# Optimization experiments

Measured on AMD Instinct MI355X. Metric: run time of the kernel, lower is better.

## Reference

```python
import jax, jax.numpy as jnp
import numpy as np

HID = 256

def setup_inputs() -> dict:
    key = jax.random.key(0)
    ks = jax.random.split(key, 16)
    B, N, DIN, DOUT = 256, 1024, 64, 128
    def lin(k, fin, fout):
        kw, kb = jax.random.split(k)
        s = 1.0 / np.sqrt(fin)
        W = jax.random.uniform(kw, (fin, fout), jnp.float32, -s, s)
        b = jax.random.uniform(kb, (fout,), jnp.float32, -s, s)
        return W, b
    x = jax.random.normal(ks[0], (B, N, DIN), jnp.float32)
    mask = jax.random.randint(ks[1], (B, N), 0, 2) > 0
    pw1, pb1 = lin(ks[2], DIN, HID)
    pw2, pb2 = lin(ks[3], HID, HID)
    pw3, pb3 = lin(ks[4], HID, HID)
    rw1, rb1 = lin(ks[5], HID, HID)
    rw2, rb2 = lin(ks[6], HID, HID)
    rw3, rb3 = lin(ks[7], HID, DOUT)
    return dict(x=x, mask=mask, pw1=pw1, pb1=pb1, pw2=pw2, pb2=pb2, pw3=pw3, pb3=pb3,
                rw1=rw1, rb1=rb1, rw2=rw2, rb2=rb2, rw3=rw3, rb3=rb3)

def reference(x, mask, pw1, pb1, pw2, pb2, pw3, pb3, rw1, rb1, rw2, rb2, rw3, rb3):
    # x: [B, N, din], mask: [B, N] bool
    # phi per element (padding elements are zeroed before the pool, matching
    # the torch pack/pad pipeline which only runs phi on valid elements)
    h = jax.nn.relu(jnp.einsum('bnd,dh->bnh', x, pw1) + pb1)
    h = jax.nn.relu(jnp.einsum('bnh,hk->bnk', h, pw2) + pb2)
    h = jnp.einsum('bnh,hk->bnk', h, pw3) + pb3
    m = mask.astype(x.dtype)[..., None]                  # [B, N, 1]
    pooled = jnp.sum(h * m, axis=1)                      # [B, 256]
    o = jax.nn.relu(pooled @ rw1 + rb1)
    o = jax.nn.relu(o @ rw2 + rb2)
    o = o @ rw3 + rb3                                    # [B, dout]
    # rows with zero valid elements get exactly 0 (torch leaves res at 0.0)
    valid = jnp.any(mask, axis=1, keepdims=True)
    return jnp.where(valid, o, jnp.zeros((), dtype=o.dtype))
```

## Files before the change

kernel.cpp:

```cpp
#include <hip/hip_runtime.h>

namespace {
constexpr int NB = 256, NN = 1024, DIN = 64, HID = 256, DOUT = 128;
constexpr int MT = 64;

typedef __attribute__((ext_vector_type(8))) short bf16x8;
typedef __attribute__((ext_vector_type(4))) float f32x4;

constexpr size_t PW1_OFF = 0;
constexpr size_t PW2_OFF = (size_t)DIN * HID * 2;

__device__ inline unsigned short f2bf(float f) {
    union { float f; unsigned u; } v; v.f = f;
    unsigned r = v.u + 0x7FFF + ((v.u >> 16) & 1);
    return (unsigned short)(r >> 16);
}

__global__ void prep(const float* __restrict__ pw1, const float* __restrict__ pw2,
                     unsigned short* __restrict__ w1p, unsigned short* __restrict__ w2p) {
    int i = blockIdx.x * 256 + threadIdx.x;
    if (i < DIN * HID / 8) {
        int s0 = i * 8;
        int k = s0 >> 8, n0 = s0 & 255;
        float4 v0 = *(const float4*)(pw1 + s0);
        float4 v1 = *(const float4*)(pw1 + s0 + 4);
        float vv[8] = {v0.x, v0.y, v0.z, v0.w, v1.x, v1.y, v1.z, v1.w};
        int j = k & 7, quad = (k >> 3) & 3, kk = k >> 5;
#pragma unroll
        for (int e = 0; e < 8; ++e) {
            int n = n0 + e, strip = n >> 4, l15 = n & 15;
            w1p[strip * 1024 + kk * 512 + (quad * 16 + l15) * 8 + j] = f2bf(vv[e]);
        }
    }
    if (i < HID * HID / 8) {
        int s0 = i * 8;
        int k = s0 >> 8, n0 = s0 & 255;
        float4 v0 = *(const float4*)(pw2 + s0);
        float4 v1 = *(const float4*)(pw2 + s0 + 4);
        float vv[8] = {v0.x, v0.y, v0.z, v0.w, v1.x, v1.y, v1.z, v1.w};
        int j = k & 7, quad = (k >> 3) & 3, kk = k >> 5;
#pragma unroll
        for (int e = 0; e < 8; ++e) {
            int n = n0 + e, strip = n >> 4, l15 = n & 15;
            w2p[strip * 4096 + kk * 512 + (quad * 16 + l15) * 8 + j] = f2bf(vv[e]);
        }
    }
}

__device__ inline float4 dotseg(const float* __restrict__ buf, const float* __restrict__ W,
                                int c, int s) {
    const float4* W4 = (const float4*)W;
    float4 acc = make_float4(0.f, 0.f, 0.f, 0.f);
#pragma unroll 8
    for (int i = 0; i < 32; ++i) {
        int k = s * 32 + i;
        float bk = buf[k];
        float4 w = W4[(size_t)k * 64 + c];
        acc.x = fmaf(bk, w.x, acc.x);
        acc.y = fmaf(bk, w.y, acc.y);
        acc.z = fmaf(bk, w.z, acc.z);
        acc.w = fmaf(bk, w.w, acc.w);
    }
    return acc;
}

__launch_bounds__(512, 2)
__global__ void deepset(const float* __restrict__ x, const int* __restrict__ mask,
                        const float* __restrict__ pb1, const float* __restrict__ pb2,
                        const unsigned short* __restrict__ w1p,
                        const unsigned short* __restrict__ w2p,
                        const float* __restrict__ pw3, const float* __restrict__ pb3,
                        const float* __restrict__ rw1, const float* __restrict__ rb1,
                        const float* __restrict__ rw2, const float* __restrict__ rb2,
                        const float* __restrict__ rw3, const float* __restrict__ rb3,
                        float* __restrict__ out)
{
    __shared__ unsigned short xs[2][MT * 64];
    __shared__ unsigned short h1s[MT * 256];
    __shared__ short vlist[NN];
    __shared__ float pooledS[HID];
    __shared__ float part[8][HID];
    __shared__ float bufB[HID], bufC[HID];
    __shared__ int cnt_s;

    const int b = blockIdx.x, t = threadIdx.x;
    const int lane = t & 63, wq = t >> 6;
    const int quad = lane >> 4, l15 = lane & 15;

    if (t == 0) cnt_s = 0;
    __syncthreads();
    if (mask[b * NN + t] != 0)       { int i = atomicAdd(&cnt_s, 1); vlist[i] = (short)t; }
    if (mask[b * NN + t + 512] != 0) { int i = atomicAdd(&cnt_s, 1); vlist[i] = (short)(t + 512); }
    __syncthreads();
    const int cnt = cnt_s;

    const uint4* w1q = (const uint4*)w1p;
    const uint4* w2q = (const uint4*)w2p;
    uint4 w1f[2][2], w2f[8][2];
#pragma unroll
    for (int j = 0; j < 2; ++j) {
        int strip = wq * 2 + j;
#pragma unroll
        for (int kk = 0; kk < 2; ++kk) w1f[kk][j] = w1q[(strip * 2 + kk) * 64 + lane];
#pragma unroll
        for (int kk = 0; kk < 8; ++kk) w2f[kk][j] = w2q[(strip * 8 + kk) * 64 + lane];
    }
    float bias1[2], bias2[2];
#pragma unroll
    for (int j = 0; j < 2; ++j) {
        int c = wq * 32 + j * 16 + l15;
        bias1[j] = pb1[c]; bias2[j] = pb2[c];
    }

    float pool[2] = {0.f, 0.f};
    const float* xb = x + (size_t)b * NN * DIN;
    const int gr = t >> 3, seg8 = t & 7;
    const int xoff = gr * 64 + ((seg8 ^ (gr & 7)) << 3);

    {
        float4 a0 = make_float4(0.f,0.f,0.f,0.f), a1 = a0;
        if (gr < min(MT, cnt)) {
            const float4* p = (const float4*)(xb + (size_t)vlist[gr] * DIN + seg8 * 8);
            a0 = p[0]; a1 = p[1];
        }
        unsigned short tmp[8] = {f2bf(a0.x),f2bf(a0.y),f2bf(a0.z),f2bf(a0.w),
                                 f2bf(a1.x),f2bf(a1.y),f2bf(a1.z),f2bf(a1.w)};
        *(uint4*)&xs[0][xoff] = *(const uint4*)tmp;
    }

    int cur = 0;
    for (int base = 0; base < cnt; base += MT) {
        __syncthreads();

        f32x4 acc[4][2];
#pragma unroll
        for (int f = 0; f < 4; ++f)
#pragma unroll
            for (int j = 0; j < 2; ++j) acc[f][j] = (f32x4){0.f,0.f,0.f,0.f};
#pragma unroll
        for (int kk = 0; kk < 2; ++kk) {
            bf16x8 a[4];
#pragma unroll
            for (int f = 0; f < 4; ++f)
                a[f] = *(const bf16x8*)&xs[cur][(f*16 + l15)*64 + (((kk*4 + quad) ^ (l15 & 7)) << 3)];
#pragma unroll
            for (int j = 0; j < 2; ++j) {
                bf16x8 bw = __builtin_bit_cast(bf16x8, w1f[kk][j]);
#pragma unroll
                for (int f = 0; f < 4; ++f)
                    acc[f][j] = __builtin_amdgcn_mfma_f32_16x16x32_bf16(a[f], bw, acc[f][j], 0, 0, 0);
            }
        }
#pragma unroll
        for (int f = 0; f < 4; ++f)
#pragma unroll
            for (int j = 0; j < 2; ++j) {
                int col = wq * 32 + j * 16 + l15, kb = col >> 3, cl = col & 7;
#pragma unroll
                for (int r = 0; r < 4; ++r) {
                    int row = f * 16 + quad * 4 + r;
                    float h = fmaxf(acc[f][j][r] + bias1[j], 0.f);
                    h1s[row * 256 + ((kb ^ (row & 7)) << 3) + cl] = f2bf(h);
                }
            }

        float4 n0 = make_float4(0.f,0.f,0.f,0.f), n1 = n0;
        const bool hn = (base + MT) < cnt;
        if (hn && gr < cnt - (base + MT)) {
            const float4* p = (const float4*)(xb + (size_t)vlist[base + MT + gr] * DIN + seg8 * 8);
            n0 = p[0]; n1 = p[1];
        }
        __syncthreads();

        f32x4 acc2[4][2];
#pragma unroll
        for (int f = 0; f < 4; ++f)
#pragma unroll
            for (int j = 0; j < 2; ++j) acc2[f][j] = (f32x4){0.f,0.f,0.f,0.f};
#pragma unroll
        for (int kk = 0; kk < 8; ++kk) {
            bf16x8 a[4];
#pragma unroll
            for (int f = 0; f < 4; ++f)
                a[f] = *(const bf16x8*)&h1s[(f*16 + l15)*256 + (((kk*4 + quad) ^ (l15 & 7)) << 3)];
#pragma unroll
            for (int j = 0; j < 2; ++j) {
                bf16x8 bw = __builtin_bit_cast(bf16x8, w2f[kk][j]);
#pragma unroll
                for (int f = 0; f < 4; ++f)
                    acc2[f][j] = __builtin_amdgcn_mfma_f32_16x16x32_bf16(a[f], bw, acc2[f][j], 0, 0, 0);
            }
        }
#pragma unroll
        for (int f = 0; f < 4; ++f)
#pragma unroll
            for (int r = 0; r < 4; ++r) {
                bool v = (base + f * 16 + quad * 4 + r) < cnt;
#pragma unroll
                for (int j = 0; j < 2; ++j) {
                    float h = fmaxf(acc2[f][j][r] + bias2[j], 0.f);
                    pool[j] += v ? h : 0.f;
                }
            }

        if (hn) {
            unsigned short tmp[8] = {f2bf(n0.x),f2bf(n0.y),f2bf(n0.z),f2bf(n0.w),
                                     f2bf(n1.x),f2bf(n1.y),f2bf(n1.z),f2bf(n1.w)};
            *(uint4*)&xs[cur ^ 1][xoff] = *(const uint4*)tmp;
        }
        cur ^= 1;
    }

#pragma unroll
    for (int j = 0; j < 2; ++j) {
        float v = pool[j];
        v += __shfl_xor(v, 16, 64);
        v += __shfl_xor(v, 32, 64);
        if (quad == 0) pooledS[wq * 32 + j * 16 + l15] = v;
    }
    __syncthreads();

    const int c = t & 63, s = t >> 6;
    {
        float4 p = dotseg(pooledS, pw3, c, s);
        ((float4*)part[s])[c] = p;
        __syncthreads();
        if (t < HID) {
            float v = (float)cnt * pb3[t];
#pragma unroll
            for (int g = 0; g < 8; ++g) v += part[g][t];
            bufB[t] = v;
        }
        __syncthreads();
    }
    {
        float4 p = dotseg(bufB, rw1, c, s);
        ((float4*)part[s])[c] = p;
        __syncthreads();
        if (t < HID) {
            float v = rb1[t];
#pragma unroll
            for (int g = 0; g < 8; ++g) v += part[g][t];
            bufC[t] = fmaxf(v, 0.f);
        }
        __syncthreads();
    }
    {
        float4 p = dotseg(bufC, rw2, c, s);
        ((float4*)part[s])[c] = p;
        __syncthreads();
        if (t < HID) {
            float v = rb2[t];
#pragma unroll
            for (int g = 0; g < 8; ++g) v += part[g][t];
            bufB[t] = fmaxf(v, 0.f);
        }
        __syncthreads();
    }
    {
        const int c4 = t & 31, s4 = t >> 5;
        const float4* W4 = (const float4*)rw3;
        float4 acc = make_float4(0.f, 0.f, 0.f, 0.f);
#pragma unroll 8
        for (int i = 0; i < 16; ++i) {
            int k = s4 * 16 + i;
            float bk = bufB[k];
            float4 w = W4[(size_t)k * 32 + c4];
            acc.x = fmaf(bk, w.x, acc.x);
            acc.y = fmaf(bk, w.y, acc.y);
            acc.z = fmaf(bk, w.z, acc.z);
            acc.w = fmaf(bk, w.w, acc.w);
        }
        float* part2 = &part[0][0];
        ((float4*)(part2 + s4 * DOUT))[c4] = acc;
        __syncthreads();
        if (t < DOUT) {
            float v = rb3[t];
#pragma unroll
            for (int g = 0; g < 16; ++g) v += part2[g * DOUT + t];
            out[b * DOUT + t] = (cnt > 0) ? v : 0.f;
        }
    }
}
}

extern "C" void kernel_launch(void* const* d_in, const int* in_sizes, int n_in,
                              void* d_out, int out_size, void* d_ws, size_t ws_size,
                              hipStream_t stream) {
    const float* x    = (const float*)d_in[0];
    const int*   mask = (const int*)  d_in[1];
    const float* pw1  = (const float*)d_in[2];
    const float* pb1  = (const float*)d_in[3];
    const float* pw2  = (const float*)d_in[4];
    const float* pb2  = (const float*)d_in[5];
    const float* pw3  = (const float*)d_in[6];
    const float* pb3  = (const float*)d_in[7];
    const float* rw1  = (const float*)d_in[8];
    const float* rb1  = (const float*)d_in[9];
    const float* rw2  = (const float*)d_in[10];
    const float* rb2  = (const float*)d_in[11];
    const float* rw3  = (const float*)d_in[12];
    const float* rb3  = (const float*)d_in[13];
    float* out = (float*)d_out;

    unsigned short* w1p = (unsigned short*)((char*)d_ws + PW1_OFF);
    unsigned short* w2p = (unsigned short*)((char*)d_ws + PW2_OFF);

    prep<<<dim3(32), dim3(256), 0, stream>>>(pw1, pw2, w1p, w2p);
    deepset<<<dim3(NB), dim3(512), 0, stream>>>(x, mask, pb1, pb2, w1p, w2p,
                                                pw3, pb3, rw1, rb1, rw2, rb2, rw3, rb3, out);
}
```

Baseline: 145.3 us.

## Split per-set phi work across two blocks and move rho to a separate kernel

The fused per-batch kernel is split into a phi_pool kernel launched on a (batch, 2) grid, where each block handles half of the set elements and accumulates pooled sums and counts with global atomics. A separate rho kernel then runs the small MLP on the pooled vectors. Spreading the work over twice as many blocks, with launch bounds raised to 4, is meant to improve occupancy and load balance across the CUs, and prep now writes the weight repack with coalesced vector stores and zeroes the accumulators. The cost is an extra kernel launch, global atomics, and a round trip of the pooled vectors through memory.

```diff
diff --git a/kernel.cpp b/kernel.cpp
--- a/kernel.cpp
+++ b/kernel.cpp
@@ -2,48 +2,202 @@
 
 namespace {
 constexpr int NB = 256, NN = 1024, DIN = 64, HID = 256, DOUT = 128;
+constexpr int SPLIT = 2, CHUNK = NN / SPLIT;
 constexpr int MT = 64;
 
 typedef __attribute__((ext_vector_type(8))) short bf16x8;
 typedef __attribute__((ext_vector_type(4))) float f32x4;
 
-constexpr size_t PW1_OFF = 0;
-constexpr size_t PW2_OFF = (size_t)DIN * HID * 2;
+constexpr size_t POOLED_OFF = 0;
+constexpr size_t CNTS_OFF   = (size_t)NB * HID * 4;
+constexpr size_t PW1_OFF    = CNTS_OFF + (size_t)NB * 4;
+constexpr size_t PW2_OFF    = PW1_OFF + (size_t)DIN * HID * 2;
+constexpr int ZERO_N = NB * HID + NB;
 
 __device__ inline unsigned short f2bf(float f) {
     union { float f; unsigned u; } v; v.f = f;
     unsigned r = v.u + 0x7FFF + ((v.u >> 16) & 1);
     return (unsigned short)(r >> 16);
 }
+__device__ inline unsigned pk2(float lo, float hi) {
+    return (unsigned)f2bf(lo) | ((unsigned)f2bf(hi) << 16);
+}
 
 __global__ void prep(const float* __restrict__ pw1, const float* __restrict__ pw2,
+                     float* __restrict__ zero_base,
                      unsigned short* __restrict__ w1p, unsigned short* __restrict__ w2p) {
     int i = blockIdx.x * 256 + threadIdx.x;
+    if (i < ZERO_N) zero_base[i] = 0.f;
     if (i < DIN * HID / 8) {
-        int s0 = i * 8;
-        int k = s0 >> 8, n0 = s0 & 255;
-        float4 v0 = *(const float4*)(pw1 + s0);
-        float4 v1 = *(const float4*)(pw1 + s0 + 4);
-        float vv[8] = {v0.x, v0.y, v0.z, v0.w, v1.x, v1.y, v1.z, v1.w};
-        int j = k & 7, quad = (k >> 3) & 3, kk = k >> 5;
-#pragma unroll
-        for (int e = 0; e < 8; ++e) {
-            int n = n0 + e, strip = n >> 4, l15 = n & 15;
-            w1p[strip * 1024 + kk * 512 + (quad * 16 + l15) * 8 + j] = f2bf(vv[e]);
-        }
+        int lane = i & 63, kk = (i >> 6) & 1, strip = i >> 7;
+        int kbase = kk * 32 + ((lane >> 4) * 8);
+        int n = strip * 16 + (lane & 15);
+        const float* src = pw1 + (size_t)kbase * HID + n;
+        float v[8];
+#pragma unroll
+        for (int j = 0; j < 8; ++j) v[j] = src[(size_t)j * HID];
+        unsigned o[4] = {pk2(v[0],v[1]), pk2(v[2],v[3]), pk2(v[4],v[5]), pk2(v[6],v[7])};
+        *(uint4*)(w1p + (size_t)i * 8) = *(const uint4*)o;
     }
     if (i < HID * HID / 8) {
-        int s0 = i * 8;
-        int k = s0 >> 8, n0 = s0 & 255;
-        float4 v0 = *(const float4*)(pw2 + s0);
-        float4 v1 = *(const float4*)(pw2 + s0 + 4);
-        float vv[8] = {v0.x, v0.y, v0.z, v0.w, v1.x, v1.y, v1.z, v1.w};
-        int j = k & 7, quad = (k >> 3) & 3, kk = k >> 5;
-#pragma unroll
-        for (int e = 0; e < 8; ++e) {
-            int n = n0 + e, strip = n >> 4, l15 = n & 15;
-            w2p[strip * 4096 + kk * 512 + (quad * 16 + l15) * 8 + j] = f2bf(vv[e]);
-        }
+        int lane = i & 63, kk = (i >> 6) & 7, strip = i >> 9;
+        int kbase = kk * 32 + ((lane >> 4) * 8);
+        int n = strip * 16 + (lane & 15);
+        const float* src = pw2 + (size_t)kbase * HID + n;
+        float v[8];
+#pragma unroll
+        for (int j = 0; j < 8; ++j) v[j] = src[(size_t)j * HID];
+        unsigned o[4] = {pk2(v[0],v[1]), pk2(v[2],v[3]), pk2(v[4],v[5]), pk2(v[6],v[7])};
+        *(uint4*)(w2p + (size_t)i * 8) = *(const uint4*)o;
+    }
+}
+
+__launch_bounds__(512, 4)
+__global__ void phi_pool(const float* __restrict__ x, const int* __restrict__ mask,
+                         const float* __restrict__ pb1, const float* __restrict__ pb2,
+                         const unsigned short* __restrict__ w1p,
+                         const unsigned short* __restrict__ w2p,
+                         float* __restrict__ pooled, int* __restrict__ cnts) {
+    __shared__ unsigned short xs[2][MT * 64];
+    __shared__ unsigned short h1s[MT * 256];
+    __shared__ short vlist[CHUNK];
+    __shared__ int cnt_s;
+
+    const int b = blockIdx.x, sp = blockIdx.y, t = threadIdx.x;
+    const int lane = t & 63, wq = t >> 6;
+    const int quad = lane >> 4, l15 = lane & 15;
+
+    if (t == 0) cnt_s = 0;
+    __syncthreads();
+    {
+        int n = sp * CHUNK + t;
+        if (mask[b * NN + n] != 0) { int i = atomicAdd(&cnt_s, 1); vlist[i] = (short)n; }
+    }
+    __syncthreads();
+    const int cnt = cnt_s;
+    if (t == 0) atomicAdd(&cnts[b], cnt);
+
+    const uint4* w1q = (const uint4*)w1p;
+    const uint4* w2q = (const uint4*)w2p;
+    uint4 w1f[2][2], w2f[8][2];
+#pragma unroll
+    for (int j = 0; j < 2; ++j) {
+        int strip = wq * 2 + j;
+#pragma unroll
+        for (int kk = 0; kk < 2; ++kk) w1f[kk][j] = w1q[(strip * 2 + kk) * 64 + lane];
+#pragma unroll
+        for (int kk = 0; kk < 8; ++kk) w2f[kk][j] = w2q[(strip * 8 + kk) * 64 + lane];
+    }
+    float bias1[2], bias2[2];
+#pragma unroll
+    for (int j = 0; j < 2; ++j) {
+        int c = wq * 32 + j * 16 + l15;
+        bias1[j] = pb1[c]; bias2[j] = pb2[c];
+    }
+
+    float pool[2] = {0.f, 0.f};
+    const float* xb = x + (size_t)b * NN * DIN;
+    const int gr = t >> 3, seg8 = t & 7;
+    const int xoff = gr * 64 + ((seg8 ^ (gr & 7)) << 3);
+
+    {
+        float4 a0 = make_float4(0.f,0.f,0.f,0.f), a1 = a0;
+        if (gr < min(MT, cnt)) {
+            const float4* p = (const float4*)(xb + (size_t)vlist[gr] * DIN + seg8 * 8);
+            a0 = p[0]; a1 = p[1];
+        }
+        unsigned o[4] = {pk2(a0.x,a0.y), pk2(a0.z,a0.w), pk2(a1.x,a1.y), pk2(a1.z,a1.w)};
+        *(uint4*)&xs[0][xoff] = *(const uint4*)o;
+    }
+
+    int cur = 0;
+    for (int base = 0; base < cnt; base += MT) {
+        __syncthreads();
+
+        f32x4 acc[4][2];
+#pragma unroll
+        for (int f = 0; f < 4; ++f)
+#pragma unroll
+            for (int j = 0; j < 2; ++j) acc[f][j] = (f32x4){0.f,0.f,0.f,0.f};
+#pragma unroll
+        for (int kk = 0; kk < 2; ++kk) {
+            bf16x8 a[4];
+#pragma unroll
+            for (int f = 0; f < 4; ++f)
+                a[f] = *(const bf16x8*)&xs[cur][(f*16 + l15)*64 + (((kk*4 + quad) ^ (l15 & 7)) << 3)];
+#pragma unroll
+            for (int j = 0; j < 2; ++j) {
+                bf16x8 bw = __builtin_bit_cast(bf16x8, w1f[kk][j]);
+#pragma unroll
+                for (int f = 0; f < 4; ++f)
+                    acc[f][j] = __builtin_amdgcn_mfma_f32_16x16x32_bf16(a[f], bw, acc[f][j], 0, 0, 0);
+            }
+        }
+#pragma unroll
+        for (int f = 0; f < 4; ++f)
+#pragma unroll
+            for (int j = 0; j < 2; ++j) {
+                int col = wq * 32 + j * 16 + l15, kb = col >> 3, cl = col & 7;
+#pragma unroll
+                for (int r = 0; r < 4; ++r) {
+                    int row = f * 16 + quad * 4 + r;
+                    float h = fmaxf(acc[f][j][r] + bias1[j], 0.f);
+                    h1s[row * 256 + ((kb ^ (row & 7)) << 3) + cl] = f2bf(h);
+                }
+            }
+
+        float4 n0 = make_float4(0.f,0.f,0.f,0.f), n1 = n0;
+        const bool hn = (base + MT) < cnt;
+        if (hn && gr < cnt - (base + MT)) {
+            const float4* p = (const float4*)(xb + (size_t)vlist[base + MT + gr] * DIN + seg8 * 8);
+            n0 = p[0]; n1 = p[1];
+        }
+        __syncthreads();
+
+        f32x4 acc2[4][2];
+#pragma unroll
+        for (int f = 0; f < 4; ++f)
+#pragma unroll
+            for (int j = 0; j < 2; ++j) acc2[f][j] = (f32x4){0.f,0.f,0.f,0.f};
+#pragma unroll
+        for (int kk = 0; kk < 8; ++kk) {
+            bf16x8 a[4];
+#pragma unroll
+            for (int f = 0; f < 4; ++f)
+                a[f] = *(const bf16x8*)&h1s[(f*16 + l15)*256 + (((kk*4 + quad) ^ (l15 & 7)) << 3)];
+#pragma unroll
+            for (int j = 0; j < 2; ++j) {
+                bf16x8 bw = __builtin_bit_cast(bf16x8, w2f[kk][j]);
+#pragma unroll
+                for (int f = 0; f < 4; ++f)
+                    acc2[f][j] = __builtin_amdgcn_mfma_f32_16x16x32_bf16(a[f], bw, acc2[f][j], 0, 0, 0);
+            }
+        }
+#pragma unroll
+        for (int f = 0; f < 4; ++f)
+#pragma unroll
+            for (int r = 0; r < 4; ++r) {
+                bool v = (base + f * 16 + quad * 4 + r) < cnt;
+#pragma unroll
+                for (int j = 0; j < 2; ++j) {
+                    float h = fmaxf(acc2[f][j][r] + bias2[j], 0.f);
+                    pool[j] += v ? h : 0.f;
+                }
+            }
+
+        if (hn) {
+            unsigned o[4] = {pk2(n0.x,n0.y), pk2(n0.z,n0.w), pk2(n1.x,n1.y), pk2(n1.z,n1.w)};
+            *(uint4*)&xs[cur ^ 1][xoff] = *(const uint4*)o;
+        }
+        cur ^= 1;
+    }
+
+#pragma unroll
+    for (int j = 0; j < 2; ++j) {
+        float v = pool[j];
+        v += __shfl_xor(v, 16, 64);
+        v += __shfl_xor(v, 32, 64);
+        if (quad == 0) atomicAdd(&pooled[b * HID + wq * 32 + j * 16 + l15], v);
     }
 }
 
@@ -65,164 +219,22 @@
 }
 
 __launch_bounds__(512, 2)
-__global__ void deepset(const float* __restrict__ x, const int* __restrict__ mask,
-                        const float* __restrict__ pb1, const float* __restrict__ pb2,
-                        const unsigned short* __restrict__ w1p,
-                        const unsigned short* __restrict__ w2p,
-                        const float* __restrict__ pw3, const float* __restrict__ pb3,
-                        const float* __restrict__ rw1, const float* __restrict__ rb1,
-                        const float* __restrict__ rw2, const float* __restrict__ rb2,
-                        const float* __restrict__ rw3, const float* __restrict__ rb3,
-                        float* __restrict__ out)
-{
-    __shared__ unsigned short xs[2][MT * 64];
-    __shared__ unsigned short h1s[MT * 256];
-    __shared__ short vlist[NN];
-    __shared__ float pooledS[HID];
+__global__ void rho(const float* __restrict__ pooled, const int* __restrict__ cnts,
+                    const float* __restrict__ pw3, const float* __restrict__ pb3,
+                    const float* __restrict__ rw1, const float* __restrict__ rb1,
+                    const float* __restrict__ rw2, const float* __restrict__ rb2,
+                    const float* __restrict__ rw3, const float* __restrict__ rb3,
+                    float* __restrict__ out) {
+    __shared__ float bufA[HID], bufB[HID];
     __shared__ float part[8][HID];
-    __shared__ float bufB[HID], bufC[HID];
-    __shared__ int cnt_s;
-
     const int b = blockIdx.x, t = threadIdx.x;
-    const int lane = t & 63, wq = t >> 6;
-    const int quad = lane >> 4, l15 = lane & 15;
-
-    if (t == 0) cnt_s = 0;
+    const int c = t & 63, s = t >> 6;
+    const int cnt = cnts[b];
+    if (t < HID) bufA[t] = pooled[b * HID + t];
     __syncthreads();
-    if (mask[b * NN + t] != 0)       { int i = atomicAdd(&cnt_s, 1); vlist[i] = (short)t; }
-    if (mask[b * NN + t + 512] != 0) { int i = atomicAdd(&cnt_s, 1); vlist[i] = (short)(t + 512); }
-    __syncthreads();
-    const int cnt = cnt_s;
-
-    const uint4* w1q = (const uint4*)w1p;
-    const uint4* w2q = (const uint4*)w2p;
-    uint4 w1f[2][2], w2f[8][2];
-#pragma unroll
-    for (int j = 0; j < 2; ++j) {
-        int strip = wq * 2 + j;
-#pragma unroll
-        for (int kk = 0; kk < 2; ++kk) w1f[kk][j] = w1q[(strip * 2 + kk) * 64 + lane];
-#pragma unroll
-        for (int kk = 0; kk < 8; ++kk) w2f[kk][j] = w2q[(strip * 8 + kk) * 64 + lane];
-    }
-    float bias1[2], bias2[2];
-#pragma unroll
-    for (int j = 0; j < 2; ++j) {
-        int c = wq * 32 + j * 16 + l15;
-        bias1[j] = pb1[c]; bias2[j] = pb2[c];
-    }
-
-    float pool[2] = {0.f, 0.f};
-    const float* xb = x + (size_t)b * NN * DIN;
-    const int gr = t >> 3, seg8 = t & 7;
-    const int xoff = gr * 64 + ((seg8 ^ (gr & 7)) << 3);
-
-    {
-        float4 a0 = make_float4(0.f,0.f,0.f,0.f), a1 = a0;
-        if (gr < min(MT, cnt)) {
-            const float4* p = (const float4*)(xb + (size_t)vlist[gr] * DIN + seg8 * 8);
-            a0 = p[0]; a1 = p[1];
-        }
-        unsigned short tmp[8] = {f2bf(a0.x),f2bf(a0.y),f2bf(a0.z),f2bf(a0.w),
-                                 f2bf(a1.x),f2bf(a1.y),f2bf(a1.z),f2bf(a1.w)};
-        *(uint4*)&xs[0][xoff] = *(const uint4*)tmp;
-    }
-
-    int cur = 0;
-    for (int base = 0; base < cnt; base += MT) {
-        __syncthreads();
-
-        f32x4 acc[4][2];
-#pragma unroll
-        for (int f = 0; f < 4; ++f)
-#pragma unroll
-            for (int j = 0; j < 2; ++j) acc[f][j] = (f32x4){0.f,0.f,0.f,0.f};
-#pragma unroll
-        for (int kk = 0; kk < 2; ++kk) {
-            bf16x8 a[4];
-#pragma unroll
-            for (int f = 0; f < 4; ++f)
-                a[f] = *(const bf16x8*)&xs[cur][(f*16 + l15)*64 + (((kk*4 + quad) ^ (l15 & 7)) << 3)];
-#pragma unroll
-            for (int j = 0; j < 2; ++j) {
-                bf16x8 bw = __builtin_bit_cast(bf16x8, w1f[kk][j]);
-#pragma unroll
-                for (int f = 0; f < 4; ++f)
-                    acc[f][j] = __builtin_amdgcn_mfma_f32_16x16x32_bf16(a[f], bw, acc[f][j], 0, 0, 0);
-            }
-        }
-#pragma unroll
-        for (int f = 0; f < 4; ++f)
-#pragma unroll
-            for (int j = 0; j < 2; ++j) {
-                int col = wq * 32 + j * 16 + l15, kb = col >> 3, cl = col & 7;
-#pragma unroll
-                for (int r = 0; r < 4; ++r) {
-                    int row = f * 16 + quad * 4 + r;
-                    float h = fmaxf(acc[f][j][r] + bias1[j], 0.f);
-                    h1s[row * 256 + ((kb ^ (row & 7)) << 3) + cl] = f2bf(h);
-                }
-            }
-
-        float4 n0 = make_float4(0.f,0.f,0.f,0.f), n1 = n0;
-        const bool hn = (base + MT) < cnt;
-        if (hn && gr < cnt - (base + MT)) {
-            const float4* p = (const float4*)(xb + (size_t)vlist[base + MT + gr] * DIN + seg8 * 8);
-            n0 = p[0]; n1 = p[1];
-        }
-        __syncthreads();
-
-        f32x4 acc2[4][2];
-#pragma unroll
-        for (int f = 0; f < 4; ++f)
-#pragma unroll
-            for (int j = 0; j < 2; ++j) acc2[f][j] = (f32x4){0.f,0.f,0.f,0.f};
-#pragma unroll
-        for (int kk = 0; kk < 8; ++kk) {
-            bf16x8 a[4];
-#pragma unroll
-            for (int f = 0; f < 4; ++f)
-                a[f] = *(const bf16x8*)&h1s[(f*16 + l15)*256 + (((kk*4 + quad) ^ (l15 & 7)) << 3)];
-#pragma unroll
-            for (int j = 0; j < 2; ++j) {
-                bf16x8 bw = __builtin_bit_cast(bf16x8, w2f[kk][j]);
-#pragma unroll
-                for (int f = 0; f < 4; ++f)
-                    acc2[f][j] = __builtin_amdgcn_mfma_f32_16x16x32_bf16(a[f], bw, acc2[f][j], 0, 0, 0);
-            }
-        }
-#pragma unroll
-        for (int f = 0; f < 4; ++f)
-#pragma unroll
-            for (int r = 0; r < 4; ++r) {
-                bool v = (base + f * 16 + quad * 4 + r) < cnt;
-#pragma unroll
-                for (int j = 0; j < 2; ++j) {
-                    float h = fmaxf(acc2[f][j][r] + bias2[j], 0.f);
-                    pool[j] += v ? h : 0.f;
-                }
-            }
-
-        if (hn) {
-            unsigned short tmp[8] = {f2bf(n0.x),f2bf(n0.y),f2bf(n0.z),f2bf(n0.w),
-                                     f2bf(n1.x),f2bf(n1.y),f2bf(n1.z),f2bf(n1.w)};
-            *(uint4*)&xs[cur ^ 1][xoff] = *(const uint4*)tmp;
-        }
-        cur ^= 1;
-    }
-
-#pragma unroll
-    for (int j = 0; j < 2; ++j) {
-        float v = pool[j];
-        v += __shfl_xor(v, 16, 64);
-        v += __shfl_xor(v, 32, 64);
-        if (quad == 0) pooledS[wq * 32 + j * 16 + l15] = v;
-    }
-    __syncthreads();
-
-    const int c = t & 63, s = t >> 6;
-    {
-        float4 p = dotseg(pooledS, pw3, c, s);
+
+    {
+        float4 p = dotseg(bufA, pw3, c, s);
         ((float4*)part[s])[c] = p;
         __syncthreads();
         if (t < HID) {
@@ -241,12 +253,12 @@
             float v = rb1[t];
 #pragma unroll
             for (int g = 0; g < 8; ++g) v += part[g][t];
-            bufC[t] = fmaxf(v, 0.f);
-        }
-        __syncthreads();
-    }
-    {
-        float4 p = dotseg(bufC, rw2, c, s);
+            bufA[t] = fmaxf(v, 0.f);
+        }
+        __syncthreads();
+    }
+    {
+        float4 p = dotseg(bufA, rw2, c, s);
         ((float4*)part[s])[c] = p;
         __syncthreads();
         if (t < HID) {
@@ -303,10 +315,13 @@
     const float* rb3  = (const float*)d_in[13];
     float* out = (float*)d_out;
 
+    float* pooled       = (float*)((char*)d_ws + POOLED_OFF);
+    int*   cnts         = (int*)  ((char*)d_ws + CNTS_OFF);
     unsigned short* w1p = (unsigned short*)((char*)d_ws + PW1_OFF);
     unsigned short* w2p = (unsigned short*)((char*)d_ws + PW2_OFF);
 
-    prep<<<dim3(32), dim3(256), 0, stream>>>(pw1, pw2, w1p, w2p);
-    deepset<<<dim3(NB), dim3(512), 0, stream>>>(x, mask, pb1, pb2, w1p, w2p,
-                                                pw3, pb3, rw1, rb1, rw2, rb2, rw3, rb3, out);
-}
+    prep<<<dim3(257), dim3(256), 0, stream>>>(pw1, pw2, (float*)d_ws, w1p, w2p);
+    phi_pool<<<dim3(NB, SPLIT), dim3(512), 0, stream>>>(x, mask, pb1, pb2, w1p, w2p, pooled, cnts);
+    rho<<<dim3(NB), dim3(512), 0, stream>>>(pooled, cnts, pw3, pb3,
+                                            rw1, rb1, rw2, rb2, rw3, rb3, out);
+}
```

New measurement: 229.8 us. 1.58x slower.
